# Kernel tuning notes

Hardware: AMD Instinct MI355X
Metric: run time of the kernel (lower is better)

## Reference

```python
import jax, jax.numpy as jnp
import numpy as np

IN_FEATURES = 128
HIDDEN_DIM = 128
ALPHA = 0.2
NEG_INF = -9e15


def setup_inputs() -> dict:
    key = jax.random.key(0)
    k1, k2, k3, k4, k5 = jax.random.split(key, 5)
    N, n_context = 20000, 32
    h_i = jax.random.normal(k1, (N, IN_FEATURES), dtype=jnp.float32)
    context_indices = jax.random.randint(k2, (N, n_context), 0, N, dtype=jnp.int64)
    # learned params (torch nn.Linear default init scale ~ U(-1/sqrt(fan_in), 1/sqrt(fan_in)))
    s1 = 1.0 / np.sqrt(IN_FEATURES)
    s2 = 1.0 / np.sqrt(2 * HIDDEN_DIM)
    W_i = jax.random.uniform(k3, (IN_FEATURES, HIDDEN_DIM), jnp.float32, -s1, s1)
    W_j = jax.random.uniform(k4, (IN_FEATURES, HIDDEN_DIM), jnp.float32, -s1, s1)
    ka, kb = jax.random.split(k5)
    a_w = jax.random.uniform(ka, (2 * HIDDEN_DIM, 1), jnp.float32, -s2, s2)
    a_b = jax.random.uniform(kb, (1,), jnp.float32, -s2, s2)
    return {"h_i": h_i, "context_indices": context_indices,
            "W_i": W_i, "W_j": W_j, "a_w": a_w, "a_b": a_b}


def reference(h_i, context_indices, W_i, W_j, a_w, a_b):
    N, n_context = context_indices.shape
    # -1 padding maps to an extra zero row (torch indexes -1 -> last row of padded table)
    h_padded = jnp.concatenate([h_i, jnp.zeros((1, h_i.shape[1]), h_i.dtype)], axis=0)
    idx = jnp.where(context_indices >= 0, context_indices, N)
    h_j = h_padded[idx]                      # [N, n_context, in_features]
    Wh_i = h_i @ W_i                         # [N, hidden]
    Wh_j = jnp.einsum('ncf,fh->nch', h_j, W_j)  # [N, n_context, hidden]
    # attention_layer(cat(Wh_i, Wh_j)) split into two matvecs (same math as concat)
    a_i, a_j = a_w[:HIDDEN_DIM, 0], a_w[HIDDEN_DIM:, 0]
    e = Wh_i @ a_i                           # [N]
    e = e[:, None] + Wh_j @ a_j + a_b[0]     # [N, n_context]
    e = jax.nn.leaky_relu(e, ALPHA)
    e = jnp.where(context_indices >= 0, e, NEG_INF)
    attn = jax.nn.softmax(e, axis=1)         # [N, n_context]
    h_prime = jnp.einsum('nc,nch->nh', attn, Wh_j)
    return h_prime
```

## Files before the change

kernel.cpp:

```cpp
#include <hip/hip_runtime.h>
#include <hip/hip_fp16.h>

#define GAT_ALPHA 0.2f
#define GAT_NEG_INF -9.0e15f

typedef _Float16 half8_t __attribute__((ext_vector_type(8)));
typedef float f32x4 __attribute__((ext_vector_type(4)));

__global__ __launch_bounds__(256) void gat_transform_mfma(
    const float* __restrict__ h, const float* __restrict__ Wi,
    const float* __restrict__ Wj, const float* __restrict__ aw,
    const float* __restrict__ ab,
    __half* __restrict__ Wh16, float* __restrict__ e1, float* __restrict__ e2,
    int N) {
    __shared__ _Float16 sWt[128 * 136];
    __shared__ float svi[128];
    const int t = threadIdx.x;

    if (t < 128) {
        const float4* wrow = (const float4*)(Wi + (size_t)t * 128);
        const float4* a4 = (const float4*)aw;
        float s = 0.f;
        #pragma unroll
        for (int i = 0; i < 32; ++i) {
            float4 w = wrow[i], a = a4[i];
            s = fmaf(w.x, a.x, s); s = fmaf(w.y, a.y, s);
            s = fmaf(w.z, a.z, s); s = fmaf(w.w, a.w, s);
        }
        svi[t] = s;
    }
    for (int i = t; i < 128 * 128; i += 256) {
        int k = i >> 7, n = i & 127;
        sWt[n * 136 + k] = (_Float16)Wj[i];
    }
    __syncthreads();

    const int wave = t >> 6, lane = t & 63, q = lane >> 4, l16 = lane & 15;
    const float abv = ab[0];

    float vir[4][8];
    #pragma unroll
    for (int s = 0; s < 4; ++s) {
        float4 u0 = *(const float4*)(svi + s * 32 + q * 8);
        float4 u1 = *(const float4*)(svi + s * 32 + q * 8 + 4);
        vir[s][0] = u0.x; vir[s][1] = u0.y; vir[s][2] = u0.z; vir[s][3] = u0.w;
        vir[s][4] = u1.x; vir[s][5] = u1.y; vir[s][6] = u1.z; vir[s][7] = u1.w;
    }
    float ajr[8];
    #pragma unroll
    for (int c = 0; c < 8; ++c) ajr[c] = aw[128 + c * 16 + l16];

    const int ntiles = (N + 15) >> 4;
    for (int tile = blockIdx.x * 4 + wave; tile < ntiles; tile += gridDim.x * 4) {
        const int base = tile << 4;
        int row = base + l16; if (row >= N) row = N - 1;
        const float* hp = h + (size_t)row * 128 + q * 8;

        half8_t af[4];
        float pe1 = 0.f;
        #pragma unroll
        for (int s = 0; s < 4; ++s) {
            float4 f0 = *(const float4*)(hp + s * 32);
            float4 f1 = *(const float4*)(hp + s * 32 + 4);
            pe1 = fmaf(f0.x, vir[s][0], pe1); pe1 = fmaf(f0.y, vir[s][1], pe1);
            pe1 = fmaf(f0.z, vir[s][2], pe1); pe1 = fmaf(f0.w, vir[s][3], pe1);
            pe1 = fmaf(f1.x, vir[s][4], pe1); pe1 = fmaf(f1.y, vir[s][5], pe1);
            pe1 = fmaf(f1.z, vir[s][6], pe1); pe1 = fmaf(f1.w, vir[s][7], pe1);
            half8_t a;
            a[0] = (_Float16)f0.x; a[1] = (_Float16)f0.y;
            a[2] = (_Float16)f0.z; a[3] = (_Float16)f0.w;
            a[4] = (_Float16)f1.x; a[5] = (_Float16)f1.y;
            a[6] = (_Float16)f1.z; a[7] = (_Float16)f1.w;
            af[s] = a;
        }

        f32x4 acc[8];
        #pragma unroll
        for (int c = 0; c < 8; ++c) { f32x4 z = {0.f, 0.f, 0.f, 0.f}; acc[c] = z; }

        const _Float16* wbase = sWt + l16 * 136 + q * 8;
        #pragma unroll
        for (int s = 0; s < 4; ++s) {
            #pragma unroll
            for (int c = 0; c < 8; ++c) {
                half8_t bf = *(const half8_t*)(wbase + c * (16 * 136) + s * 32);
                acc[c] = __builtin_amdgcn_mfma_f32_16x16x32_f16(af[s], bf, acc[c], 0, 0, 0);
            }
        }

        const bool full = (base + 16 <= N);
        float pe2[4] = {0.f, 0.f, 0.f, 0.f};
        #pragma unroll
        for (int c = 0; c < 8; ++c) {
            #pragma unroll
            for (int r = 0; r < 4; ++r) {
                float v = acc[c][r];
                pe2[r] = fmaf(v, ajr[c], pe2[r]);
                int rr = base + q * 4 + r;
                if (full || rr < N)
                    Wh16[(size_t)rr * 128 + (c * 16 + l16)] = __float2half(v);
            }
        }
        #pragma unroll
        for (int r = 0; r < 4; ++r) {
            pe2[r] += __shfl_xor(pe2[r], 1);
            pe2[r] += __shfl_xor(pe2[r], 2);
            pe2[r] += __shfl_xor(pe2[r], 4);
            pe2[r] += __shfl_xor(pe2[r], 8);
        }
        if (l16 == 0) {
            #pragma unroll
            for (int r = 0; r < 4; ++r) {
                int rr = base + q * 4 + r;
                if (rr < N) e2[rr] = pe2[r];
            }
        }
        pe1 += __shfl_xor(pe1, 16);
        pe1 += __shfl_xor(pe1, 32);
        if (lane < 16) {
            int rr = base + lane;
            if (rr < N) e1[rr] = pe1 + abv;
        }
    }
}

__global__ __launch_bounds__(256, 8) void gat_gather1(
    const int* __restrict__ ctx, const float* __restrict__ e1,
    const float* __restrict__ e2, const __half* __restrict__ Wh16,
    float* __restrict__ out, int N) {
    const int t = threadIdx.x;
    const int wave = t >> 6, lane = t & 63;
    const int qq = lane >> 4, ll = lane & 15;
    const int n = blockIdx.x * 4 + wave;
    if (n >= N) return;

    const int c32 = lane & 31;
    const int j = ctx[(size_t)n * 32 + c32];
    const bool v = (j >= 0);
    const int jj = v ? j : 0;
    const float eb = e1[n];
    float lg = eb + e2[jj];
    lg = fmaxf(lg, GAT_ALPHA * lg);
    lg = v ? lg : GAT_NEG_INF;
    float m = lg;
    #pragma unroll
    for (int s = 16; s; s >>= 1) m = fmaxf(m, __shfl_xor(m, s, 32));
    float p = v ? __expf(lg - m) : 0.f;
    float ss = p;
    #pragma unroll
    for (int s = 16; s; s >>= 1) ss += __shfl_xor(ss, s, 32);
    const float inv = (ss > 0.f) ? __frcp_rn(ss) : 0.f;
    p *= inv;
    const int o = jj << 8;

    float a0 = 0.f, a1 = 0.f, a2 = 0.f, a3 = 0.f;
    float a4 = 0.f, a5 = 0.f, a6 = 0.f, a7 = 0.f;
    const char* wb = (const char*)Wh16 + (size_t)(ll * 16);
    #pragma unroll
    for (int k = 0; k < 8; ++k) {
        const int src = qq * 8 + k;
        const float w = __shfl(p, src, 32);
        const int  off = __shfl(o, src, 32);
        half8_t hv = *(const half8_t*)(wb + off);
        a0 = fmaf(w, (float)hv[0], a0); a1 = fmaf(w, (float)hv[1], a1);
        a2 = fmaf(w, (float)hv[2], a2); a3 = fmaf(w, (float)hv[3], a3);
        a4 = fmaf(w, (float)hv[4], a4); a5 = fmaf(w, (float)hv[5], a5);
        a6 = fmaf(w, (float)hv[6], a6); a7 = fmaf(w, (float)hv[7], a7);
    }
    a0 += __shfl_xor(a0, 16); a1 += __shfl_xor(a1, 16);
    a2 += __shfl_xor(a2, 16); a3 += __shfl_xor(a3, 16);
    a4 += __shfl_xor(a4, 16); a5 += __shfl_xor(a5, 16);
    a6 += __shfl_xor(a6, 16); a7 += __shfl_xor(a7, 16);
    a0 += __shfl_xor(a0, 32); a1 += __shfl_xor(a1, 32);
    a2 += __shfl_xor(a2, 32); a3 += __shfl_xor(a3, 32);
    a4 += __shfl_xor(a4, 32); a5 += __shfl_xor(a5, 32);
    a6 += __shfl_xor(a6, 32); a7 += __shfl_xor(a7, 32);

    if (lane < 16) {
        float4* orow = (float4*)(out + (size_t)n * 128);
        float4 u; u.x = a0; u.y = a1; u.z = a2; u.w = a3;
        float4 w2; w2.x = a4; w2.y = a5; w2.z = a6; w2.w = a7;
        orow[2 * ll] = u;
        orow[2 * ll + 1] = w2;
    }
}

extern "C" void kernel_launch(void* const* d_in, const int* in_sizes, int n_in,
                              void* d_out, int out_size, void* d_ws, size_t ws_size,
                              hipStream_t stream) {
    const float* h   = (const float*)d_in[0];
    const int*   ctx = (const int*)d_in[1];
    const float* Wi  = (const float*)d_in[2];
    const float* Wj  = (const float*)d_in[3];
    const float* aw  = (const float*)d_in[4];
    const float* ab  = (const float*)d_in[5];
    float* out = (float*)d_out;
    const int N = in_sizes[0] / 128;

    float* e1 = (float*)d_ws;
    float* e2 = e1 + N;
    __half* Wh16 = (__half*)(e2 + N);

    const int ntiles = (N + 15) >> 4;
    const int g1 = (ntiles + 3) / 4;
    const int g2 = (N + 3) / 4;

    gat_transform_mfma<<<g1, 256, 0, stream>>>(h, Wi, Wj, aw, ab, Wh16, e1, e2, N);
    gat_gather1<<<g2, 256, 0, stream>>>(ctx, e1, e2, Wh16, out, N);
}
```

Measured before the change: 102.3 us.

## Compute neighbor attention logits inside gather from gathered Wh rows

The transform kernel no longer computes or stores the e2 vector. The gather kernel now computes each neighbor's logit as a dot of the fp16 Wh row it already loads with a_j. This removes the separate dependent e2 gather before the softmax, lets all eight neighbor row loads issue up front, and defers normalization to one multiply at the output. In exchange it adds per-neighbor dot products with shuffle reductions, uses fp16-rounded Wh for the logits (a small precision change), lowers the occupancy hint to 4, and adds nontemporal loads and stores.

```diff
diff --git a/kernel.cpp b/kernel.cpp
--- a/kernel.cpp
+++ b/kernel.cpp
@@ -11,8 +11,7 @@
     const float* __restrict__ h, const float* __restrict__ Wi,
     const float* __restrict__ Wj, const float* __restrict__ aw,
     const float* __restrict__ ab,
-    __half* __restrict__ Wh16, float* __restrict__ e1, float* __restrict__ e2,
-    int N) {
+    __half* __restrict__ Wh16, float* __restrict__ e1, int N) {
     __shared__ _Float16 sWt[128 * 136];
     __shared__ float svi[128];
     const int t = threadIdx.x;
@@ -46,9 +45,6 @@
         vir[s][0] = u0.x; vir[s][1] = u0.y; vir[s][2] = u0.z; vir[s][3] = u0.w;
         vir[s][4] = u1.x; vir[s][5] = u1.y; vir[s][6] = u1.z; vir[s][7] = u1.w;
     }
-    float ajr[8];
-    #pragma unroll
-    for (int c = 0; c < 8; ++c) ajr[c] = aw[128 + c * 16 + l16];
 
     const int ntiles = (N + 15) >> 4;
     for (int tile = blockIdx.x * 4 + wave; tile < ntiles; tile += gridDim.x * 4) {
@@ -89,30 +85,13 @@
         }
 
         const bool full = (base + 16 <= N);
-        float pe2[4] = {0.f, 0.f, 0.f, 0.f};
         #pragma unroll
         for (int c = 0; c < 8; ++c) {
             #pragma unroll
             for (int r = 0; r < 4; ++r) {
-                float v = acc[c][r];
-                pe2[r] = fmaf(v, ajr[c], pe2[r]);
                 int rr = base + q * 4 + r;
                 if (full || rr < N)
-                    Wh16[(size_t)rr * 128 + (c * 16 + l16)] = __float2half(v);
-            }
-        }
-        #pragma unroll
-        for (int r = 0; r < 4; ++r) {
-            pe2[r] += __shfl_xor(pe2[r], 1);
-            pe2[r] += __shfl_xor(pe2[r], 2);
-            pe2[r] += __shfl_xor(pe2[r], 4);
-            pe2[r] += __shfl_xor(pe2[r], 8);
-        }
-        if (l16 == 0) {
-            #pragma unroll
-            for (int r = 0; r < 4; ++r) {
-                int rr = base + q * 4 + r;
-                if (rr < N) e2[rr] = pe2[r];
+                    Wh16[(size_t)rr * 128 + (c * 16 + l16)] = __float2half(acc[c][r]);
             }
         }
         pe1 += __shfl_xor(pe1, 16);
@@ -124,9 +103,9 @@
     }
 }
 
-__global__ __launch_bounds__(256, 8) void gat_gather1(
+__global__ __launch_bounds__(256, 4) void gat_gather_fused(
     const int* __restrict__ ctx, const float* __restrict__ e1,
-    const float* __restrict__ e2, const __half* __restrict__ Wh16,
+    const float* __restrict__ aw, const __half* __restrict__ Wh16,
     float* __restrict__ out, int N) {
     const int t = threadIdx.x;
     const int wave = t >> 6, lane = t & 63;
@@ -135,38 +114,80 @@
     if (n >= N) return;
 
     const int c32 = lane & 31;
-    const int j = ctx[(size_t)n * 32 + c32];
-    const bool v = (j >= 0);
-    const int jj = v ? j : 0;
+    const int j = __builtin_nontemporal_load(ctx + (size_t)n * 32 + c32);
     const float eb = e1[n];
-    float lg = eb + e2[jj];
-    lg = fmaxf(lg, GAT_ALPHA * lg);
-    lg = v ? lg : GAT_NEG_INF;
-    float m = lg;
-    #pragma unroll
-    for (int s = 16; s; s >>= 1) m = fmaxf(m, __shfl_xor(m, s, 32));
-    float p = v ? __expf(lg - m) : 0.f;
-    float ss = p;
-    #pragma unroll
-    for (int s = 16; s; s >>= 1) ss += __shfl_xor(ss, s, 32);
+
+    const int qb = qq * 8;
+    const int j0 = __shfl(j, qb + 0, 32);
+    const int j1 = __shfl(j, qb + 1, 32);
+    const int j2 = __shfl(j, qb + 2, 32);
+    const int j3 = __shfl(j, qb + 3, 32);
+    const int j4 = __shfl(j, qb + 4, 32);
+    const int j5 = __shfl(j, qb + 5, 32);
+    const int j6 = __shfl(j, qb + 6, 32);
+    const int j7 = __shfl(j, qb + 7, 32);
+    const bool v0 = j0 >= 0, v1 = j1 >= 0, v2 = j2 >= 0, v3 = j3 >= 0;
+    const bool v4 = j4 >= 0, v5 = j5 >= 0, v6 = j6 >= 0, v7 = j7 >= 0;
+
+    const char* wb = (const char*)Wh16 + (size_t)(ll * 16);
+    half8_t hv0 = *(const half8_t*)(wb + ((v0 ? j0 : 0) << 8));
+    half8_t hv1 = *(const half8_t*)(wb + ((v1 ? j1 : 0) << 8));
+    half8_t hv2 = *(const half8_t*)(wb + ((v2 ? j2 : 0) << 8));
+    half8_t hv3 = *(const half8_t*)(wb + ((v3 ? j3 : 0) << 8));
+    half8_t hv4 = *(const half8_t*)(wb + ((v4 ? j4 : 0) << 8));
+    half8_t hv5 = *(const half8_t*)(wb + ((v5 ? j5 : 0) << 8));
+    half8_t hv6 = *(const half8_t*)(wb + ((v6 ? j6 : 0) << 8));
+    half8_t hv7 = *(const half8_t*)(wb + ((v7 ? j7 : 0) << 8));
+
+    const float4 aj0 = *(const float4*)(aw + 128 + ll * 8);
+    const float4 aj1 = *(const float4*)(aw + 128 + ll * 8 + 4);
+
+#define GAT_DOT(HV, D)                                                     \
+    float D = fmaf((float)HV[0], aj0.x, 0.f);                              \
+    D = fmaf((float)HV[1], aj0.y, D); D = fmaf((float)HV[2], aj0.z, D);    \
+    D = fmaf((float)HV[3], aj0.w, D); D = fmaf((float)HV[4], aj1.x, D);    \
+    D = fmaf((float)HV[5], aj1.y, D); D = fmaf((float)HV[6], aj1.z, D);    \
+    D = fmaf((float)HV[7], aj1.w, D);                                      \
+    D += __shfl_xor(D, 1, 16); D += __shfl_xor(D, 2, 16);                  \
+    D += __shfl_xor(D, 4, 16); D += __shfl_xor(D, 8, 16);
+    GAT_DOT(hv0, d0) GAT_DOT(hv1, d1) GAT_DOT(hv2, d2) GAT_DOT(hv3, d3)
+    GAT_DOT(hv4, d4) GAT_DOT(hv5, d5) GAT_DOT(hv6, d6) GAT_DOT(hv7, d7)
+#undef GAT_DOT
+
+#define GAT_LG(D, V)                                                       \
+    D = eb + D; D = fmaxf(D, GAT_ALPHA * D); D = V ? D : GAT_NEG_INF;
+    GAT_LG(d0, v0) GAT_LG(d1, v1) GAT_LG(d2, v2) GAT_LG(d3, v3)
+    GAT_LG(d4, v4) GAT_LG(d5, v5) GAT_LG(d6, v6) GAT_LG(d7, v7)
+#undef GAT_LG
+
+    float m = fmaxf(fmaxf(fmaxf(d0, d1), fmaxf(d2, d3)),
+                    fmaxf(fmaxf(d4, d5), fmaxf(d6, d7)));
+    m = fmaxf(m, __shfl_xor(m, 16));
+    m = fmaxf(m, __shfl_xor(m, 32));
+    const float p0 = v0 ? __expf(d0 - m) : 0.f;
+    const float p1 = v1 ? __expf(d1 - m) : 0.f;
+    const float p2 = v2 ? __expf(d2 - m) : 0.f;
+    const float p3 = v3 ? __expf(d3 - m) : 0.f;
+    const float p4 = v4 ? __expf(d4 - m) : 0.f;
+    const float p5 = v5 ? __expf(d5 - m) : 0.f;
+    const float p6 = v6 ? __expf(d6 - m) : 0.f;
+    const float p7 = v7 ? __expf(d7 - m) : 0.f;
+    float ss = ((p0 + p1) + (p2 + p3)) + ((p4 + p5) + (p6 + p7));
+    ss += __shfl_xor(ss, 16);
+    ss += __shfl_xor(ss, 32);
     const float inv = (ss > 0.f) ? __frcp_rn(ss) : 0.f;
-    p *= inv;
-    const int o = jj << 8;
 
     float a0 = 0.f, a1 = 0.f, a2 = 0.f, a3 = 0.f;
     float a4 = 0.f, a5 = 0.f, a6 = 0.f, a7 = 0.f;
-    const char* wb = (const char*)Wh16 + (size_t)(ll * 16);
-    #pragma unroll
-    for (int k = 0; k < 8; ++k) {
-        const int src = qq * 8 + k;
-        const float w = __shfl(p, src, 32);
-        const int  off = __shfl(o, src, 32);
-        half8_t hv = *(const half8_t*)(wb + off);
-        a0 = fmaf(w, (float)hv[0], a0); a1 = fmaf(w, (float)hv[1], a1);
-        a2 = fmaf(w, (float)hv[2], a2); a3 = fmaf(w, (float)hv[3], a3);
-        a4 = fmaf(w, (float)hv[4], a4); a5 = fmaf(w, (float)hv[5], a5);
-        a6 = fmaf(w, (float)hv[6], a6); a7 = fmaf(w, (float)hv[7], a7);
-    }
+#define GAT_ACC(HV, W)                                                     \
+    a0 = fmaf(W, (float)HV[0], a0); a1 = fmaf(W, (float)HV[1], a1);        \
+    a2 = fmaf(W, (float)HV[2], a2); a3 = fmaf(W, (float)HV[3], a3);        \
+    a4 = fmaf(W, (float)HV[4], a4); a5 = fmaf(W, (float)HV[5], a5);        \
+    a6 = fmaf(W, (float)HV[6], a6); a7 = fmaf(W, (float)HV[7], a7);
+    GAT_ACC(hv0, p0) GAT_ACC(hv1, p1) GAT_ACC(hv2, p2) GAT_ACC(hv3, p3)
+    GAT_ACC(hv4, p4) GAT_ACC(hv5, p5) GAT_ACC(hv6, p6) GAT_ACC(hv7, p7)
+#undef GAT_ACC
+
     a0 += __shfl_xor(a0, 16); a1 += __shfl_xor(a1, 16);
     a2 += __shfl_xor(a2, 16); a3 += __shfl_xor(a3, 16);
     a4 += __shfl_xor(a4, 16); a5 += __shfl_xor(a5, 16);
@@ -177,11 +198,13 @@
     a6 += __shfl_xor(a6, 32); a7 += __shfl_xor(a7, 32);
 
     if (lane < 16) {
-        float4* orow = (float4*)(out + (size_t)n * 128);
-        float4 u; u.x = a0; u.y = a1; u.z = a2; u.w = a3;
-        float4 w2; w2.x = a4; w2.y = a5; w2.z = a6; w2.w = a7;
-        orow[2 * ll] = u;
-        orow[2 * ll + 1] = w2;
+        f32x4 u; u[0] = a0 * inv; u[1] = a1 * inv;
+        u[2] = a2 * inv; u[3] = a3 * inv;
+        f32x4 w2; w2[0] = a4 * inv; w2[1] = a5 * inv;
+        w2[2] = a6 * inv; w2[3] = a7 * inv;
+        f32x4* orow = (f32x4*)(out + (size_t)n * 128) + 2 * ll;
+        __builtin_nontemporal_store(u, orow);
+        __builtin_nontemporal_store(w2, orow + 1);
     }
 }
 
@@ -197,14 +220,14 @@
     float* out = (float*)d_out;
     const int N = in_sizes[0] / 128;
 
+    const int Npad = (N + 7) & ~7;
     float* e1 = (float*)d_ws;
-    float* e2 = e1 + N;
-    __half* Wh16 = (__half*)(e2 + N);
+    __half* Wh16 = (__half*)(e1 + Npad);
 
     const int ntiles = (N + 15) >> 4;
     const int g1 = (ntiles + 3) / 4;
     const int g2 = (N + 3) / 4;
 
-    gat_transform_mfma<<<g1, 256, 0, stream>>>(h, Wi, Wj, aw, ab, Wh16, e1, e2, N);
-    gat_gather1<<<g2, 256, 0, stream>>>(ctx, e1, e2, Wh16, out, N);
+    gat_transform_mfma<<<g1, 256, 0, stream>>>(h, Wi, Wj, aw, ab, Wh16, e1, N);
+    gat_gather_fused<<<g2, 256, 0, stream>>>(ctx, e1, aw, Wh16, out, N);
 }
```

Result: slower. 105.5 us (+3.1%).
